# Performance work log

Measured on AMD Instinct MI355X. Metric: run time of the kernel, lower is better.

Reference implementation:

```python
import jax, jax.numpy as jnp
import numpy as np

K = 6  # knn_number
EPS_CS = 1e-8  # F.cosine_similarity eps


def _sqdist(a, b):
    # a: [B,N,3], b: [B,M,3] -> [B,N,M] squared euclidean distances
    return (jnp.sum(a * a, -1)[:, :, None]
            + jnp.sum(b * b, -1)[:, None, :]
            - 2.0 * jnp.einsum('bnc,bmc->bnm', a, b))


def _batch_norm(x):
    # normalize last dim with the module's exact epsilons
    n = jnp.sqrt(jnp.sum(x * x, axis=-1, keepdims=True) + 1e-08)
    return x / (n + 1e-10)


def _cossim(a, b):
    # torch F.cosine_similarity semantics along last dim
    na = jnp.maximum(jnp.sqrt(jnp.sum(a * a, -1)), EPS_CS)
    nb = jnp.maximum(jnp.sqrt(jnp.sum(b * b, -1)), EPS_CS)
    return jnp.sum(a * b, -1) / (na * nb)


def _gather(points, idx):
    # points: [B,N,C], idx: [B,...] int -> [B,...,C]
    return jax.vmap(lambda p, i: p[i])(points, idx)


def _avg_ori(group_ori, group_nor, batch_ori, batch_nor):
    # group_*: [B,N,K,3], batch_*: [B,N,3]
    nor_diff = jnp.sum(group_nor * batch_nor[:, :, None, :], axis=3)  # [B,N,K]
    nor_diff = jnp.exp(-nor_diff / 0.3) * 10.0 + 1.0
    nor_diff = jnp.where(nor_diff < 4.0, 1.0, 5.0)
    batch_ori_rot = jnp.cross(batch_ori, batch_nor)  # get_ori_rot90: ori x nor
    cos0 = _cossim(group_ori, batch_ori[:, :, None, :])       # [B,N,K]
    cos1 = _cossim(group_ori, batch_ori_rot[:, :, None, :])   # [B,N,K]
    cos = jnp.minimum(1.0 - jnp.abs(cos0), 1.0 - jnp.abs(cos1))
    return jnp.mean(nor_diff * cos)


def _forward(ori_pre, nor_pre, xyz_up, xyz_offset, pts, gt):
    ori_pre = _batch_norm(ori_pre)
    nor_pre = _batch_norm(nor_pre)
    xyz_gt = gt[:, :, 0:3]
    xyz_nor = gt[:, :, 3:6]

    # ori-loss: NN of pts in gt, gather gt normals
    index = jnp.argmin(_sqdist(pts, xyz_gt), axis=2)  # [B,N]
    nor_gt = _gather(xyz_nor, index)                  # [B,N,3]
    d_n = jnp.sum(nor_gt * ori_pre, axis=2, keepdims=True)
    ori_pro = _batch_norm(ori_pre - nor_gt * d_n)

    # smooth field over KNN (self-knn over pts, includes self)
    idx = jax.lax.top_k(-_sqdist(pts, pts), K)[1]  # [B,N,K]
    group_ori = _gather(ori_pro, idx)              # [B,N,K,3]
    group_nor = _gather(nor_gt, idx)
    loss_smooth = _avg_ori(group_ori, group_nor, ori_pro, nor_gt)

    # normal estimation loss
    loss_nor = jnp.mean(1.0 - jnp.abs(_cossim(nor_gt, nor_pre)))

    # chamfer distances (squared-dist chamfer)
    do = _sqdist(xyz_offset, xyz_gt)
    loss_charm_offset = jnp.mean(jnp.min(do, axis=2)) + jnp.mean(jnp.min(do, axis=1))
    du = _sqdist(xyz_up, xyz_gt)
    loss_charm = jnp.mean(jnp.min(du, axis=2)) + jnp.mean(jnp.min(du, axis=1))

    # nor-ori orthogonality
    loss_nor_ori = jnp.mean(jnp.abs(jnp.sum(ori_pre * nor_gt, axis=2)))

    loss_cd = loss_charm + 0.4 * loss_charm_offset
    loss = loss_smooth + loss_nor + 0.1 * loss_nor_ori + 200.0 * loss_cd
    return (loss, loss_smooth, loss_nor, loss_charm_offset, loss_nor_ori, loss_charm, loss_charm)


def setup_inputs() -> dict:
    key = jax.random.key(0)
    k = jax.random.split(key, 6)
    B, N, NG, NU = 4, 4096, 4096, 8192
    gt_xyz = jax.random.normal(k[5], (B, NG, 3), dtype=jnp.float32)
    gt_nor = _batch_norm(jax.random.normal(jax.random.fold_in(key, 7), (B, NG, 3), dtype=jnp.float32))
    return {
        'ori_pre': jax.random.normal(k[0], (B, N, 3), dtype=jnp.float32),
        'nor_pre': jax.random.normal(k[1], (B, N, 3), dtype=jnp.float32),
        'xyz_up': jax.random.normal(k[2], (B, NU, 3), dtype=jnp.float32),
        'xyz_offset': jax.random.normal(k[3], (B, NU, 3), dtype=jnp.float32),
        'pts': jax.random.normal(k[4], (B, N, 3), dtype=jnp.float32),
        'gt': jnp.concatenate([gt_xyz, gt_nor], axis=-1),
        'epoch': 1,
    }


def reference(ori_pre, nor_pre, xyz_up, xyz_offset, pts, gt, epoch):
    # epoch is unused by the original forward as well
    return _forward(ori_pre, nor_pre, xyz_up, xyz_offset, pts, gt)
```

## Files before the change

### kernel.cpp

```cpp
#include <hip/hip_runtime.h>
#include <stdint.h>

#define NN 4096
#define NGG 4096
#define NUU 8192

__device__ __forceinline__ unsigned fkey32(float f) {
  unsigned u = __float_as_uint(f);
  return u ^ (((int)u >> 31) | 0x80000000u);
}
__device__ __forceinline__ float unfkey32(unsigned k) {
  unsigned m = (k & 0x80000000u) ? 0x80000000u : 0xFFFFFFFFu;
  return __uint_as_float(k ^ m);
}

__device__ __forceinline__ float block_sum_512(float v, float* sbuf) {
#pragma unroll
  for (int o = 32; o > 0; o >>= 1) v += __shfl_down(v, o, 64);
  int lane = threadIdx.x & 63;
  int w = threadIdx.x >> 6;
  if (lane == 0) sbuf[w] = v;
  __syncthreads();
  float r = 0.f;
  if (threadIdx.x == 0) {
#pragma unroll
    for (int i = 0; i < 8; ++i) r += sbuf[i];
  }
  __syncthreads();
  return r;
}

__global__ __launch_bounds__(256) void k_scan(const float* __restrict__ pts,
                                              const float* __restrict__ gt,
                                              const float* __restrict__ up,
                                              const float* __restrict__ off,
                                              unsigned long long* __restrict__ keys,
                                              unsigned* __restrict__ rowmin,
                                              unsigned* __restrict__ colmin,
                                              float* __restrict__ acc) {
  __shared__ float4 sc[512];
  int blk = blockIdx.x;
  int tid = threadIdx.x;
  if (blk == 0 && tid < 16) acc[tid] = 0.f;

  if (blk < 512) {
    int qb = blk >> 3;
    int seg = blk & 7;
    int wb = qb >> 3;
    int which = wb >> 2;
    int b = wb & 3;
    int r0 = (qb & 7) * 1024 + tid * 4;
    {
      const float* gtb = gt + (size_t)b * NGG * 6 + (size_t)seg * 512 * 6;
      int i0 = tid * 2;
      const float4* g4 = (const float4*)(gtb + (size_t)i0 * 6);
      float4 u0 = g4[0], u1 = g4[1], u2 = g4[2];
      sc[i0] = make_float4(u0.x, u0.y, u0.z,
                           fmaf(u0.x, u0.x, fmaf(u0.y, u0.y, u0.z * u0.z)));
      sc[i0 + 1] = make_float4(u1.z, u1.w, u2.x,
                               fmaf(u1.z, u1.z, fmaf(u1.w, u1.w, u2.x * u2.x)));
    }
    const float* src = which ? up : off;
    const float4* s4 = (const float4*)src;
    size_t fb = ((size_t)(b * NUU + r0) * 3) >> 2;
    float4 A = s4[fb], B = s4[fb + 1], C = s4[fb + 2];
    float q0x = A.x, q0y = A.y, q0z = A.z;
    float q1x = A.w, q1y = B.x, q1z = B.y;
    float q2x = B.z, q2y = B.w, q2z = C.x;
    float q3x = C.y, q3y = C.z, q3z = C.w;
    float qq0 = fmaf(q0x, q0x, fmaf(q0y, q0y, q0z * q0z));
    float qq1 = fmaf(q1x, q1x, fmaf(q1y, q1y, q1z * q1z));
    float qq2 = fmaf(q2x, q2x, fmaf(q2y, q2y, q2z * q2z));
    float qq3 = fmaf(q3x, q3x, fmaf(q3y, q3y, q3z * q3z));
    float a0x = -2.f * q0x, a0y = -2.f * q0y, a0z = -2.f * q0z;
    float a1x = -2.f * q1x, a1y = -2.f * q1y, a1z = -2.f * q1z;
    float a2x = -2.f * q2x, a2y = -2.f * q2y, a2z = -2.f * q2z;
    float a3x = -2.f * q3x, a3y = -2.f * q3y, a3z = -2.f * q3z;
    __syncthreads();
    float b0 = 3.4e38f, b1 = 3.4e38f, b2 = 3.4e38f, b3 = 3.4e38f;
#pragma unroll 4
    for (int j = 0; j < 512; ++j) {
      float4 c = sc[j];
      float t;
      t = fmaf(c.x, a0x, c.w); t = fmaf(c.y, a0y, t); t = fmaf(c.z, a0z, t); b0 = fminf(b0, t);
      t = fmaf(c.x, a1x, c.w); t = fmaf(c.y, a1y, t); t = fmaf(c.z, a1z, t); b1 = fminf(b1, t);
      t = fmaf(c.x, a2x, c.w); t = fmaf(c.y, a2y, t); t = fmaf(c.z, a2z, t); b2 = fminf(b2, t);
      t = fmaf(c.x, a3x, c.w); t = fmaf(c.y, a3y, t); t = fmaf(c.z, a3z, t); b3 = fminf(b3, t);
    }
    int gr = which * 32768 + b * NUU + r0;
    atomicMin(&rowmin[gr + 0], fkey32(b0 + qq0));
    atomicMin(&rowmin[gr + 1], fkey32(b1 + qq1));
    atomicMin(&rowmin[gr + 2], fkey32(b2 + qq2));
    atomicMin(&rowmin[gr + 3], fkey32(b3 + qq3));

  } else if (blk < 1024) {
    int blk2 = blk - 512;
    int qb = blk2 >> 4;
    int seg = blk2 & 15;
    int which = qb >> 4;
    int b = (qb >> 2) & 3;
    int m0 = (qb & 3) * 1024 + tid * 4;
    const float* src = which ? up : off;
    if (tid < 128) {
      const float* sb = src + (size_t)b * NUU * 3 + (size_t)seg * 512 * 3;
      int i0 = tid * 4;
      const float4* s4 = (const float4*)(sb + (size_t)i0 * 3);
      float4 u0 = s4[0], u1 = s4[1], u2 = s4[2];
      sc[i0] = make_float4(u0.x, u0.y, u0.z,
                           fmaf(u0.x, u0.x, fmaf(u0.y, u0.y, u0.z * u0.z)));
      sc[i0 + 1] = make_float4(u0.w, u1.x, u1.y,
                               fmaf(u0.w, u0.w, fmaf(u1.x, u1.x, u1.y * u1.y)));
      sc[i0 + 2] = make_float4(u1.z, u1.w, u2.x,
                               fmaf(u1.z, u1.z, fmaf(u1.w, u1.w, u2.x * u2.x)));
      sc[i0 + 3] = make_float4(u2.y, u2.z, u2.w,
                               fmaf(u2.y, u2.y, fmaf(u2.z, u2.z, u2.w * u2.w)));
    }
    const float* g = gt + (size_t)b * NGG * 6 + (size_t)m0 * 6;
    float q0x = g[0],  q0y = g[1],  q0z = g[2];
    float q1x = g[6],  q1y = g[7],  q1z = g[8];
    float q2x = g[12], q2y = g[13], q2z = g[14];
    float q3x = g[18], q3y = g[19], q3z = g[20];
    float qq0 = fmaf(q0x, q0x, fmaf(q0y, q0y, q0z * q0z));
    float qq1 = fmaf(q1x, q1x, fmaf(q1y, q1y, q1z * q1z));
    float qq2 = fmaf(q2x, q2x, fmaf(q2y, q2y, q2z * q2z));
    float qq3 = fmaf(q3x, q3x, fmaf(q3y, q3y, q3z * q3z));
    float a0x = -2.f * q0x, a0y = -2.f * q0y, a0z = -2.f * q0z;
    float a1x = -2.f * q1x, a1y = -2.f * q1y, a1z = -2.f * q1z;
    float a2x = -2.f * q2x, a2y = -2.f * q2y, a2z = -2.f * q2z;
    float a3x = -2.f * q3x, a3y = -2.f * q3y, a3z = -2.f * q3z;
    __syncthreads();
    float b0 = 3.4e38f, b1 = 3.4e38f, b2 = 3.4e38f, b3 = 3.4e38f;
#pragma unroll 4
    for (int j = 0; j < 512; ++j) {
      float4 c = sc[j];
      float t;
      t = fmaf(c.x, a0x, c.w); t = fmaf(c.y, a0y, t); t = fmaf(c.z, a0z, t); b0 = fminf(b0, t);
      t = fmaf(c.x, a1x, c.w); t = fmaf(c.y, a1y, t); t = fmaf(c.z, a1z, t); b1 = fminf(b1, t);
      t = fmaf(c.x, a2x, c.w); t = fmaf(c.y, a2y, t); t = fmaf(c.z, a2z, t); b2 = fminf(b2, t);
      t = fmaf(c.x, a3x, c.w); t = fmaf(c.y, a3y, t); t = fmaf(c.z, a3z, t); b3 = fminf(b3, t);
    }
    int gc = which * 16384 + b * NGG + m0;
    atomicMin(&colmin[gc + 0], fkey32(b0 + qq0));
    atomicMin(&colmin[gc + 1], fkey32(b1 + qq1));
    atomicMin(&colmin[gc + 2], fkey32(b2 + qq2));
    atomicMin(&colmin[gc + 3], fkey32(b3 + qq3));

  } else {
    int blk3 = blk - 1024;
    int qb = blk3 >> 4;
    int seg = blk3 & 15;
    int b = qb >> 2;
    int m0 = (qb & 3) * 1024 + tid * 4;
    if (tid < 128) {
      const float* gtb = gt + (size_t)b * NGG * 6 + (size_t)seg * 256 * 6;
      int i0 = tid * 2;
      const float4* g4 = (const float4*)(gtb + (size_t)i0 * 6);
      float4 u0 = g4[0], u1 = g4[1], u2 = g4[2];
      sc[i0] = make_float4(u0.x, u0.y, u0.z,
                           fmaf(u0.x, u0.x, fmaf(u0.y, u0.y, u0.z * u0.z)));
      sc[i0 + 1] = make_float4(u1.z, u1.w, u2.x,
                               fmaf(u1.z, u1.z, fmaf(u1.w, u1.w, u2.x * u2.x)));
    }
    size_t fb = ((size_t)(b * NN + m0) * 3) >> 2;
    const float4* p4 = (const float4*)pts;
    float4 A = p4[fb], B = p4[fb + 1], C = p4[fb + 2];
    float q0x = A.x, q0y = A.y, q0z = A.z;
    float q1x = A.w, q1y = B.x, q1z = B.y;
    float q2x = B.z, q2y = B.w, q2z = C.x;
    float q3x = C.y, q3y = C.z, q3z = C.w;
    float a0x = -2.f * q0x, a0y = -2.f * q0y, a0z = -2.f * q0z;
    float a1x = -2.f * q1x, a1y = -2.f * q1y, a1z = -2.f * q1z;
    float a2x = -2.f * q2x, a2y = -2.f * q2y, a2z = -2.f * q2z;
    float a3x = -2.f * q3x, a3y = -2.f * q3y, a3z = -2.f * q3z;
    __syncthreads();
    float b0 = 3.4e38f, b1 = 3.4e38f, b2 = 3.4e38f, b3 = 3.4e38f;
    int i0 = 0, i1 = 0, i2 = 0, i3 = 0;
#pragma unroll 4
    for (int j = 0; j < 256; ++j) {
      float4 c = sc[j];
      float t; bool cc;
      t = fmaf(c.x, a0x, c.w); t = fmaf(c.y, a0y, t); t = fmaf(c.z, a0z, t);
      cc = t < b0; b0 = cc ? t : b0; i0 = cc ? j : i0;
      t = fmaf(c.x, a1x, c.w); t = fmaf(c.y, a1y, t); t = fmaf(c.z, a1z, t);
      cc = t < b1; b1 = cc ? t : b1; i1 = cc ? j : i1;
      t = fmaf(c.x, a2x, c.w); t = fmaf(c.y, a2y, t); t = fmaf(c.z, a2z, t);
      cc = t < b2; b2 = cc ? t : b2; i2 = cc ? j : i2;
      t = fmaf(c.x, a3x, c.w); t = fmaf(c.y, a3y, t); t = fmaf(c.z, a3z, t);
      cc = t < b3; b3 = cc ? t : b3; i3 = cc ? j : i3;
    }
    int q = b * NN + m0;
    int base = seg * 256;
    atomicMin(&keys[q + 0], ((unsigned long long)fkey32(b0) << 32) | (unsigned)(base + i0));
    atomicMin(&keys[q + 1], ((unsigned long long)fkey32(b1) << 32) | (unsigned)(base + i1));
    atomicMin(&keys[q + 2], ((unsigned long long)fkey32(b2) << 32) | (unsigned)(base + i2));
    atomicMin(&keys[q + 3], ((unsigned long long)fkey32(b3) << 32) | (unsigned)(base + i3));
  }
}

#define PROJ_ORI(GIDX, NGX, NGY, NGZ, BOX, BOY, BOZ)                          \
  {                                                                           \
    unsigned idq_ = (unsigned)(keys[GIDX] & 0xffffffffULL);                   \
    const float* g_ = gt + (size_t)b * NGG * 6 + (size_t)idq_ * 6 + 3;        \
    NGX = g_[0]; NGY = g_[1]; NGZ = g_[2];                                    \
    float ox_ = ori_pre[(GIDX) * 3 + 0], oy_ = ori_pre[(GIDX) * 3 + 1],       \
          oz_ = ori_pre[(GIDX) * 3 + 2];                                      \
    float n1_ = sqrtf(fmaf(ox_, ox_, fmaf(oy_, oy_, oz_ * oz_)) + 1e-8f) +    \
                1e-10f;                                                       \
    ox_ /= n1_; oy_ /= n1_; oz_ /= n1_;                                       \
    float dn_ = fmaf(NGX, ox_, fmaf(NGY, oy_, NGZ * oz_));                    \
    float vx_ = ox_ - NGX * dn_, vy_ = oy_ - NGY * dn_, vz_ = oz_ - NGZ * dn_;\
    float n3_ = sqrtf(fmaf(vx_, vx_, fmaf(vy_, vy_, vz_ * vz_)) + 1e-8f) +    \
                1e-10f;                                                       \
    BOX = vx_ / n3_; BOY = vy_ / n3_; BOZ = vz_ / n3_;                        \
  }

#define EV(i, QX, QY, QZ) \
  fmaf(c##i##z, (QZ), fmaf(c##i##y, (QY), fmaf(c##i##x, (QX), c##i##w)))

#define MIN8Q(QX, QY, QZ) \
  fminf(fminf(fminf(EV(0, QX, QY, QZ), EV(1, QX, QY, QZ)),                    \
              fminf(EV(2, QX, QY, QZ), EV(3, QX, QY, QZ))),                   \
        fminf(fminf(EV(4, QX, QY, QZ), EV(5, QX, QY, QZ)),                    \
              fminf(EV(6, QX, QY, QZ), EV(7, QX, QY, QZ))))

#define WREDMIN(M)                                            \
  {                                                           \
    M = fminf(M, __shfl_xor(M, 32, 64));                      \
    M = fminf(M, __shfl_xor(M, 16, 64));                      \
    M = fminf(M, __shfl_xor(M, 8, 64));                       \
    M = fminf(M, __shfl_xor(M, 4, 64));                       \
    M = fminf(M, __shfl_xor(M, 2, 64));                      \
    M = fminf(M, __shfl_xor(M, 1, 64));                       \
  }

#define PUSH1(QI, E, IDX)                                                     \
  if ((E) <= tq) {                                                            \
    unsigned sl = atomicAdd(&scnt[QI], 1u);                                   \
    if (sl < 96)                                                              \
      surv[QI][sl] = ((unsigned long long)fkey32(E) << 32) | (unsigned)(IDX); \
  }

#define PASSB_Q(QI, QX, QY, QZ)                                               \
  {                                                                           \
    float tq = stau[QI];                                                      \
    float e0 = EV(0, QX, QY, QZ), e1 = EV(1, QX, QY, QZ);                     \
    float e2 = EV(2, QX, QY, QZ), e3 = EV(3, QX, QY, QZ);                     \
    float e4 = EV(4, QX, QY, QZ), e5 = EV(5, QX, QY, QZ);                     \
    float e6 = EV(6, QX, QY, QZ), e7 = EV(7, QX, QY, QZ);                     \
    float mm = fminf(fminf(fminf(e0, e1), fminf(e2, e3)),                     \
                     fminf(fminf(e4, e5), fminf(e6, e7)));                    \
    if (mm <= tq) {                                                           \
      int base = tid * 8;                                                     \
      PUSH1(QI, e0, base + 0) PUSH1(QI, e1, base + 1)                         \
      PUSH1(QI, e2, base + 2) PUSH1(QI, e3, base + 3)                         \
      PUSH1(QI, e4, base + 4) PUSH1(QI, e5, base + 5)                         \
      PUSH1(QI, e6, base + 6) PUSH1(QI, e7, base + 7)                         \
    }                                                                         \
  }

#define TAUC(VI)                                                              \
  {                                                                           \
    int nct = (v0 <= (VI)) + (v1 <= (VI)) + (v2 <= (VI)) + (v3 <= (VI)) +     \
              (v4 <= (VI)) + (v5 <= (VI)) + (v6 <= (VI)) + (v7 <= (VI));      \
    if (nct >= 6) tau = fminf(tau, (VI));                                     \
  }

__global__ __launch_bounds__(512, 4) void k_final(const float* __restrict__ pts,
                                                  const float* __restrict__ gt,
                                                  const float* __restrict__ ori_pre,
                                                  const float* __restrict__ nor_pre,
                                                  const unsigned* __restrict__ rowmin,
                                                  const unsigned* __restrict__ colmin,
                                                  const unsigned long long* __restrict__ keys,
                                                  float* __restrict__ acc,
                                                  float* __restrict__ out) {
  __shared__ unsigned long long surv[16][96];
  __shared__ unsigned scnt[16];
  __shared__ float wmin[8][16];
  __shared__ float stau[16];
  __shared__ float sred[8];
  int tid = threadIdx.x;
  int blk = blockIdx.x;

  if (blk < 1024) {
    int lane = tid & 63;
    int wave = tid >> 6;
    int b = blk >> 8;
    const float* pb = pts + (size_t)b * NN * 3;
    const float* pq = pb + (size_t)((blk & 255) * 16) * 3;

    if (tid < 16) scnt[tid] = 0;

    float c0x, c0y, c0z, c0w, c1x, c1y, c1z, c1w, c2x, c2y, c2z, c2w,
        c3x, c3y, c3z, c3w, c4x, c4y, c4z, c4w, c5x, c5y, c5z, c5w,
        c6x, c6y, c6z, c6w, c7x, c7y, c7z, c7w;
    {
      const float4* p4 = (const float4*)(pb + (size_t)tid * 24);
      float4 u0 = p4[0], u1 = p4[1], u2 = p4[2], u3 = p4[3], u4 = p4[4], u5 = p4[5];
      c0x = u0.x; c0y = u0.y; c0z = u0.z;
      c1x = u0.w; c1y = u1.x; c1z = u1.y;
      c2x = u1.z; c2y = u1.w; c2z = u2.x;
      c3x = u2.y; c3y = u2.z; c3z = u2.w;
      c4x = u3.x; c4y = u3.y; c4z = u3.z;
      c5x = u3.w; c5y = u4.x; c5z = u4.y;
      c6x = u4.z; c6y = u4.w; c6z = u5.x;
      c7x = u5.y; c7y = u5.z; c7z = u5.w;
      c0w = fmaf(c0x, c0x, fmaf(c0y, c0y, c0z * c0z));
      c1w = fmaf(c1x, c1x, fmaf(c1y, c1y, c1z * c1z));
      c2w = fmaf(c2x, c2x, fmaf(c2y, c2y, c2z * c2z));
      c3w = fmaf(c3x, c3x, fmaf(c3y, c3y, c3z * c3z));
      c4w = fmaf(c4x, c4x, fmaf(c4y, c4y, c4z * c4z));
      c5w = fmaf(c5x, c5x, fmaf(c5y, c5y, c5z * c5z));
      c6w = fmaf(c6x, c6x, fmaf(c6y, c6y, c6z * c6z));
      c7w = fmaf(c7x, c7x, fmaf(c7y, c7y, c7z * c7z));
    }

    for (int ch = 0; ch < 4; ++ch) {
      const float* qp = pq + ch * 12;
      float Q0x = -2.f * qp[0],  Q0y = -2.f * qp[1],  Q0z = -2.f * qp[2];
      float Q1x = -2.f * qp[3],  Q1y = -2.f * qp[4],  Q1z = -2.f * qp[5];
      float Q2x = -2.f * qp[6],  Q2y = -2.f * qp[7],  Q2z = -2.f * qp[8];
      float Q3x = -2.f * qp[9],  Q3y = -2.f * qp[10], Q3z = -2.f * qp[11];
      float m0 = MIN8Q(Q0x, Q0y, Q0z);
      float m1 = MIN8Q(Q1x, Q1y, Q1z);
      float m2 = MIN8Q(Q2x, Q2y, Q2z);
      float m3 = MIN8Q(Q3x, Q3y, Q3z);
      WREDMIN(m0) WREDMIN(m1) WREDMIN(m2) WREDMIN(m3)
      if (lane == 0) {
        wmin[wave][ch * 4 + 0] = m0;
        wmin[wave][ch * 4 + 1] = m1;
        wmin[wave][ch * 4 + 2] = m2;
        wmin[wave][ch * 4 + 3] = m3;
      }
    }
    __syncthreads();

    if (tid < 16) {
      float v0 = wmin[0][tid], v1 = wmin[1][tid], v2 = wmin[2][tid],
            v3 = wmin[3][tid], v4 = wmin[4][tid], v5 = wmin[5][tid],
            v6 = wmin[6][tid], v7 = wmin[7][tid];
      float tau = 3.4e38f;
      TAUC(v0) TAUC(v1) TAUC(v2) TAUC(v3) TAUC(v4) TAUC(v5) TAUC(v6) TAUC(v7)
      stau[tid] = tau;
    }
    __syncthreads();

    for (int ch = 0; ch < 4; ++ch) {
      const float* qp = pq + ch * 12;
      float Q0x = -2.f * qp[0],  Q0y = -2.f * qp[1],  Q0z = -2.f * qp[2];
      float Q1x = -2.f * qp[3],  Q1y = -2.f * qp[4],  Q1z = -2.f * qp[5];
      float Q2x = -2.f * qp[6],  Q2y = -2.f * qp[7],  Q2z = -2.f * qp[8];
      float Q3x = -2.f * qp[9],  Q3y = -2.f * qp[10], Q3z = -2.f * qp[11];
      PASSB_Q(ch * 4 + 0, Q0x, Q0y, Q0z)
      PASSB_Q(ch * 4 + 1, Q1x, Q1y, Q1z)
      PASSB_Q(ch * 4 + 2, Q2x, Q2y, Q2z)
      PASSB_Q(ch * 4 + 3, Q3x, Q3y, Q3z)
    }
    __syncthreads();

    int q_local = tid >> 5;
    int t = tid & 31;
    int q = blk * 16 + q_local;
    unsigned cnt = scnt[q_local];
    if (cnt > 96) cnt = 96;
    unsigned long long l0 = ~0ULL, l1 = ~0ULL, l2 = ~0ULL;
    for (int i = t; i < (int)cnt; i += 32) {
      unsigned long long k = surv[q_local][i];
      bool cc; unsigned long long nk;
      cc = k < l0; nk = cc ? k : l0; k = cc ? l0 : k; l0 = nk;
      cc = k < l1; nk = cc ? k : l1; k = cc ? l1 : k; l1 = nk;
      cc = k < l2; nk = cc ? k : l2;                  l2 = nk;
    }
    int myid = 0;
#pragma unroll
    for (int r = 0; r < 6; ++r) {
      unsigned long long h = l0, mk = l0;
#pragma unroll
      for (int o = 16; o > 0; o >>= 1) {
        unsigned long long other = __shfl_xor(mk, o, 32);
        mk = (other < mk) ? other : mk;
      }
      if (t == r) myid = (int)(mk & 0xffffffffULL);
      if (h == mk) { l0 = l1; l1 = l2; l2 = ~0ULL; }
    }

    float sum = 0.f;
    if (t < 6) {
      float ngx, ngy, ngz, box, boy, boz;
      PROJ_ORI(q, ngx, ngy, ngz, box, boy, boz)
      int nb = b * 4096 + myid;
      float gnx, gny, gnz, gox, goy, goz;
      PROJ_ORI(nb, gnx, gny, gnz, gox, goy, goz)
      float rx = boy * ngz - boz * ngy;
      float ry = boz * ngx - box * ngz;
      float rz = box * ngy - boy * ngx;
      float nbo = fmaxf(sqrtf(fmaf(box, box, fmaf(boy, boy, boz * boz))), 1e-8f);
      float nrot = fmaxf(sqrtf(fmaf(rx, rx, fmaf(ry, ry, rz * rz))), 1e-8f);
      float ndv = fmaf(gnx, ngx, fmaf(gny, ngy, gnz * ngz));
      float wv = (expf(-ndv / 0.3f) * 10.f + 1.f) < 4.f ? 1.f : 5.f;
      float ngo = fmaxf(sqrtf(fmaf(gox, gox, fmaf(goy, goy, goz * goz))), 1e-8f);
      float c0 = fmaf(gox, box, fmaf(goy, boy, goz * boz)) / (ngo * nbo);
      float c1 = fmaf(gox, rx, fmaf(goy, ry, goz * rz)) / (ngo * nrot);
      float cosv = fminf(1.f - fabsf(c0), 1.f - fabsf(c1));
      sum = wv * cosv;
    }
    float s = block_sum_512(sum, sred);
    if (tid == 0) atomicAdd(&acc[0], s);

  } else if (blk < 1152) {
    int i = (blk - 1024) * 512 + tid;
    float v = unfkey32(rowmin[i]);
    int slot = (i >> 15) ? 5 : 3;
    float s = block_sum_512(v, sred);
    if (tid == 0) atomicAdd(&acc[slot], s);
  } else if (blk < 1216) {
    int i = (blk - 1152) * 512 + tid;
    float v = unfkey32(colmin[i]);
    int slot = (i >> 14) ? 6 : 4;
    float s = block_sum_512(v, sred);
    if (tid == 0) atomicAdd(&acc[slot], s);
  } else {
    int q = (blk - 1216) * 512 + tid;
    int b = q >> 12;
    float ox = ori_pre[q * 3 + 0], oy = ori_pre[q * 3 + 1], oz = ori_pre[q * 3 + 2];
    float n1 = sqrtf(fmaf(ox, ox, fmaf(oy, oy, oz * oz)) + 1e-8f) + 1e-10f;
    ox /= n1; oy /= n1; oz /= n1;
    float px = nor_pre[q * 3 + 0], py = nor_pre[q * 3 + 1], pz = nor_pre[q * 3 + 2];
    float n2 = sqrtf(fmaf(px, px, fmaf(py, py, pz * pz)) + 1e-8f) + 1e-10f;
    px /= n2; py /= n2; pz /= n2;
    unsigned idx = (unsigned)(keys[q] & 0xffffffffULL);
    const float* g = gt + (size_t)b * NGG * 6 + (size_t)idx * 6 + 3;
    float gx = g[0], gy = g[1], gz = g[2];
    float dn = fmaf(gx, ox, fmaf(gy, oy, gz * oz));
    float na = fmaxf(sqrtf(fmaf(gx, gx, fmaf(gy, gy, gz * gz))), 1e-8f);
    float nb = fmaxf(sqrtf(fmaf(px, px, fmaf(py, py, pz * pz))), 1e-8f);
    float cs = fmaf(gx, px, fmaf(gy, py, gz * pz)) / (na * nb);
    float t_nor = 1.f - fabsf(cs);
    float t_ori = fabsf(dn);
    float s1 = block_sum_512(t_nor, sred);
    float s2 = block_sum_512(t_ori, sred);
    if (tid == 0) {
      atomicAdd(&acc[1], s1);
      atomicAdd(&acc[2], s2);
    }
  }

  if (tid == 0) {
    __threadfence();
    unsigned c = atomicAdd((unsigned*)(acc + 9), 1u);
    if (c == gridDim.x - 1) {
      __threadfence();
      float a0 = atomicAdd(&acc[0], 0.f);
      float a1 = atomicAdd(&acc[1], 0.f);
      float a2 = atomicAdd(&acc[2], 0.f);
      float a3 = atomicAdd(&acc[3], 0.f);
      float a4 = atomicAdd(&acc[4], 0.f);
      float a5 = atomicAdd(&acc[5], 0.f);
      float a6 = atomicAdd(&acc[6], 0.f);
      float loss_smooth = a0 / 98304.f;
      float loss_nor = a1 / 16384.f;
      float loss_nor_ori = a2 / 16384.f;
      float lco = a3 / 32768.f + a4 / 16384.f;
      float lc = a5 / 32768.f + a6 / 16384.f;
      float loss_cd = lc + 0.4f * lco;
      float loss = loss_smooth + loss_nor + 0.1f * loss_nor_ori + 200.f * loss_cd;
      out[0] = loss;
      out[1] = loss_smooth;
      out[2] = loss_nor;
      out[3] = lco;
      out[4] = loss_nor_ori;
      out[5] = lc;
      out[6] = lc;
    }
  }
}

extern "C" void kernel_launch(void* const* d_in, const int* in_sizes, int n_in,
                              void* d_out, int out_size, void* d_ws, size_t ws_size,
                              hipStream_t stream) {
  (void)in_sizes; (void)n_in; (void)out_size; (void)ws_size;
  const float* ori_pre = (const float*)d_in[0];
  const float* nor_pre = (const float*)d_in[1];
  const float* xyz_up = (const float*)d_in[2];
  const float* xyz_off = (const float*)d_in[3];
  const float* pts = (const float*)d_in[4];
  const float* gt = (const float*)d_in[5];
  float* out = (float*)d_out;
  char* ws = (char*)d_ws;

  float* acc = (float*)(ws + 0);
  unsigned long long* keys = (unsigned long long*)(ws + 512);
  unsigned* rowmin = (unsigned*)(ws + 512 + 131072);
  unsigned* colmin = (unsigned*)(ws + 512 + 131072 + 262144);

  hipMemsetAsync(ws + 512, 0xFF, 131072 + 262144 + 131072, stream);

  k_scan<<<1280, 256, 0, stream>>>(pts, gt, xyz_up, xyz_off, keys, rowmin,
                                   colmin, acc);
  k_final<<<1248, 512, 0, stream>>>(pts, gt, ori_pre, nor_pre, rowmin, colmin,
                                    keys, acc, out);
}
```

Before: 171.8 us.

## Replace atomic min reductions with per-segment partial buffers reduced in final kernel

Instead of atomicMin into shared row/col/key arrays, each scan block writes its segment's partial minima to a dedicated slice of workspace. The final kernel reduces the 8 or 16 partial slices per element when it reads them. This removes the memset launch and the contention from global atomics. In exchange it writes and reads several times more workspace memory, and the knn path now pays 16 extra key loads per gathered index.

```diff
diff --git a/kernel.cpp b/kernel.cpp
--- a/kernel.cpp
+++ b/kernel.cpp
@@ -8,10 +8,6 @@
 __device__ __forceinline__ unsigned fkey32(float f) {
   unsigned u = __float_as_uint(f);
   return u ^ (((int)u >> 31) | 0x80000000u);
-}
-__device__ __forceinline__ float unfkey32(unsigned k) {
-  unsigned m = (k & 0x80000000u) ? 0x80000000u : 0xFFFFFFFFu;
-  return __uint_as_float(k ^ m);
 }
 
 __device__ __forceinline__ float block_sum_512(float v, float* sbuf) {
@@ -30,13 +26,24 @@
   return r;
 }
 
+__device__ __forceinline__ unsigned long long key_reduce(
+    const unsigned long long* __restrict__ keysp, int q) {
+  unsigned long long mk = keysp[q];
+#pragma unroll
+  for (int s = 1; s < 16; ++s) {
+    unsigned long long v = keysp[(size_t)s * 16384 + q];
+    mk = (v < mk) ? v : mk;
+  }
+  return mk;
+}
+
 __global__ __launch_bounds__(256) void k_scan(const float* __restrict__ pts,
                                               const float* __restrict__ gt,
                                               const float* __restrict__ up,
                                               const float* __restrict__ off,
-                                              unsigned long long* __restrict__ keys,
-                                              unsigned* __restrict__ rowmin,
-                                              unsigned* __restrict__ colmin,
+                                              unsigned long long* __restrict__ keysp,
+                                              float* __restrict__ rowp,
+                                              float* __restrict__ colp,
                                               float* __restrict__ acc) {
   __shared__ float4 sc[512];
   int blk = blockIdx.x;
@@ -88,10 +95,8 @@
       t = fmaf(c.x, a3x, c.w); t = fmaf(c.y, a3y, t); t = fmaf(c.z, a3z, t); b3 = fminf(b3, t);
     }
     int gr = which * 32768 + b * NUU + r0;
-    atomicMin(&rowmin[gr + 0], fkey32(b0 + qq0));
-    atomicMin(&rowmin[gr + 1], fkey32(b1 + qq1));
-    atomicMin(&rowmin[gr + 2], fkey32(b2 + qq2));
-    atomicMin(&rowmin[gr + 3], fkey32(b3 + qq3));
+    *(float4*)(rowp + (size_t)seg * 65536 + gr) =
+        make_float4(b0 + qq0, b1 + qq1, b2 + qq2, b3 + qq3);
 
   } else if (blk < 1024) {
     int blk2 = blk - 512;
@@ -140,10 +145,8 @@
       t = fmaf(c.x, a3x, c.w); t = fmaf(c.y, a3y, t); t = fmaf(c.z, a3z, t); b3 = fminf(b3, t);
     }
     int gc = which * 16384 + b * NGG + m0;
-    atomicMin(&colmin[gc + 0], fkey32(b0 + qq0));
-    atomicMin(&colmin[gc + 1], fkey32(b1 + qq1));
-    atomicMin(&colmin[gc + 2], fkey32(b2 + qq2));
-    atomicMin(&colmin[gc + 3], fkey32(b3 + qq3));
+    *(float4*)(colp + (size_t)seg * 32768 + gc) =
+        make_float4(b0 + qq0, b1 + qq1, b2 + qq2, b3 + qq3);
 
   } else {
     int blk3 = blk - 1024;
@@ -190,16 +193,17 @@
     }
     int q = b * NN + m0;
     int base = seg * 256;
-    atomicMin(&keys[q + 0], ((unsigned long long)fkey32(b0) << 32) | (unsigned)(base + i0));
-    atomicMin(&keys[q + 1], ((unsigned long long)fkey32(b1) << 32) | (unsigned)(base + i1));
-    atomicMin(&keys[q + 2], ((unsigned long long)fkey32(b2) << 32) | (unsigned)(base + i2));
-    atomicMin(&keys[q + 3], ((unsigned long long)fkey32(b3) << 32) | (unsigned)(base + i3));
+    unsigned long long* kp = keysp + (size_t)seg * 16384 + q;
+    kp[0] = ((unsigned long long)fkey32(b0) << 32) | (unsigned)(base + i0);
+    kp[1] = ((unsigned long long)fkey32(b1) << 32) | (unsigned)(base + i1);
+    kp[2] = ((unsigned long long)fkey32(b2) << 32) | (unsigned)(base + i2);
+    kp[3] = ((unsigned long long)fkey32(b3) << 32) | (unsigned)(base + i3);
   }
 }
 
 #define PROJ_ORI(GIDX, NGX, NGY, NGZ, BOX, BOY, BOZ)                          \
   {                                                                           \
-    unsigned idq_ = (unsigned)(keys[GIDX] & 0xffffffffULL);                   \
+    unsigned idq_ = (unsigned)(key_reduce(keysp, GIDX) & 0xffffffffULL);      \
     const float* g_ = gt + (size_t)b * NGG * 6 + (size_t)idq_ * 6 + 3;        \
     NGX = g_[0]; NGY = g_[1]; NGZ = g_[2];                                    \
     float ox_ = ori_pre[(GIDX) * 3 + 0], oy_ = ori_pre[(GIDX) * 3 + 1],       \
@@ -229,7 +233,7 @@
     M = fminf(M, __shfl_xor(M, 16, 64));                      \
     M = fminf(M, __shfl_xor(M, 8, 64));                       \
     M = fminf(M, __shfl_xor(M, 4, 64));                       \
-    M = fminf(M, __shfl_xor(M, 2, 64));                      \
+    M = fminf(M, __shfl_xor(M, 2, 64));                       \
     M = fminf(M, __shfl_xor(M, 1, 64));                       \
   }
 
@@ -269,9 +273,9 @@
                                                   const float* __restrict__ gt,
                                                   const float* __restrict__ ori_pre,
                                                   const float* __restrict__ nor_pre,
-                                                  const unsigned* __restrict__ rowmin,
-                                                  const unsigned* __restrict__ colmin,
-                                                  const unsigned long long* __restrict__ keys,
+                                                  const float* __restrict__ rowp,
+                                                  const float* __restrict__ colp,
+                                                  const unsigned long long* __restrict__ keysp,
                                                   float* __restrict__ acc,
                                                   float* __restrict__ out) {
   __shared__ unsigned long long surv[16][96];
@@ -409,13 +413,19 @@
 
   } else if (blk < 1152) {
     int i = (blk - 1024) * 512 + tid;
-    float v = unfkey32(rowmin[i]);
+    float v = rowp[i];
+#pragma unroll
+    for (int sgi = 1; sgi < 8; ++sgi)
+      v = fminf(v, rowp[(size_t)sgi * 65536 + i]);
     int slot = (i >> 15) ? 5 : 3;
     float s = block_sum_512(v, sred);
     if (tid == 0) atomicAdd(&acc[slot], s);
   } else if (blk < 1216) {
     int i = (blk - 1152) * 512 + tid;
-    float v = unfkey32(colmin[i]);
+    float v = colp[i];
+#pragma unroll
+    for (int sgi = 1; sgi < 16; ++sgi)
+      v = fminf(v, colp[(size_t)sgi * 32768 + i]);
     int slot = (i >> 14) ? 6 : 4;
     float s = block_sum_512(v, sred);
     if (tid == 0) atomicAdd(&acc[slot], s);
@@ -428,7 +438,7 @@
     float px = nor_pre[q * 3 + 0], py = nor_pre[q * 3 + 1], pz = nor_pre[q * 3 + 2];
     float n2 = sqrtf(fmaf(px, px, fmaf(py, py, pz * pz)) + 1e-8f) + 1e-10f;
     px /= n2; py /= n2; pz /= n2;
-    unsigned idx = (unsigned)(keys[q] & 0xffffffffULL);
+    unsigned idx = (unsigned)(key_reduce(keysp, q) & 0xffffffffULL);
     const float* g = gt + (size_t)b * NGG * 6 + (size_t)idx * 6 + 3;
     float gx = g[0], gy = g[1], gz = g[2];
     float dn = fmaf(gx, ox, fmaf(gy, oy, gz * oz));
@@ -489,14 +499,12 @@
   char* ws = (char*)d_ws;
 
   float* acc = (float*)(ws + 0);
-  unsigned long long* keys = (unsigned long long*)(ws + 512);
-  unsigned* rowmin = (unsigned*)(ws + 512 + 131072);
-  unsigned* colmin = (unsigned*)(ws + 512 + 131072 + 262144);
-
-  hipMemsetAsync(ws + 512, 0xFF, 131072 + 262144 + 131072, stream);
-
-  k_scan<<<1280, 256, 0, stream>>>(pts, gt, xyz_up, xyz_off, keys, rowmin,
-                                   colmin, acc);
-  k_final<<<1248, 512, 0, stream>>>(pts, gt, ori_pre, nor_pre, rowmin, colmin,
-                                    keys, acc, out);
+  unsigned long long* keysp = (unsigned long long*)(ws + 512);
+  float* rowp = (float*)(ws + 512 + 2097152);
+  float* colp = (float*)(ws + 512 + 2097152 + 2097152);
+
+  k_scan<<<1280, 256, 0, stream>>>(pts, gt, xyz_up, xyz_off, keysp, rowp,
+                                   colp, acc);
+  k_final<<<1248, 512, 0, stream>>>(pts, gt, ori_pre, nor_pre, rowp, colp,
+                                    keysp, acc, out);
 }
```

Measured after the change: 179.3 us. 1.04x slower.
